# Performance work log

Hardware: AMD Instinct MI355X
Metric: run time of the kernel (lower is better)

## Reference

```python
import jax, jax.numpy as jnp
import numpy as np

N_NODES = 100000
N_EDGES = 1600000
NFEAT, NHID, NCLASS = 256, 512, 256


def _init_params(key):
    ks = jax.random.split(key, 8)
    s = 0.02
    p = {
        'W1a': jax.random.normal(ks[0], (NFEAT, NHID), jnp.float32) * s,
        'b1a': jnp.zeros((NHID,), jnp.float32),
        'W1b': jax.random.normal(ks[1], (NHID, NHID), jnp.float32) * s,
        'b1b': jnp.zeros((NHID,), jnp.float32),
        'W2a': jax.random.normal(ks[2], (NHID, NHID), jnp.float32) * s,
        'b2a': jnp.zeros((NHID,), jnp.float32),
        'W2b': jax.random.normal(ks[3], (NHID, NCLASS), jnp.float32) * s,
        'b2b': jnp.zeros((NCLASS,), jnp.float32),
        'eps1': jnp.zeros((), jnp.float32),
        'eps2': jnp.zeros((), jnp.float32),
    }
    return p


def setup_inputs() -> dict:
    key = jax.random.key(0)
    kx, ke, kp = jax.random.split(key, 3)
    x = jax.random.normal(kx, (N_NODES, NFEAT), jnp.float32)
    edge_index = jax.random.randint(ke, (2, N_EDGES), 0, N_NODES, jnp.int64)
    inp = {'x': x, 'edge_index': edge_index}
    inp.update(_init_params(kp))
    return inp


def _gin_agg(h, src, dst, eps, n_nodes):
    # sum of neighbor (source) features at each destination node + (1+eps)*self
    agg = jax.ops.segment_sum(h[src], dst, num_segments=n_nodes)
    return (1.0 + eps) * h + agg


def reference(x, edge_index, W1a, b1a, W1b, b1b, W2a, b2a, W2b, b2b, eps1, eps2):
    src, dst = edge_index[0], edge_index[1]
    n = x.shape[0]
    # GINConv layer 1: MLP = Linear-ReLU-Linear-ReLU
    h = _gin_agg(x, src, dst, eps1, n)
    h = jax.nn.relu(h @ W1a + b1a)
    h = jax.nn.relu(h @ W1b + b1b)
    # dropout: eval mode (identity)
    # GINConv layer 2: MLP = Linear-ReLU-Linear
    h = _gin_agg(h, src, dst, eps2, n)
    h = jax.nn.relu(h @ W2a + b2a)
    out = h @ W2b + b2b
    return out
```

## Files before the change

kernel.cpp:

```cpp
#include <hip/hip_runtime.h>
#include <hip/hip_bf16.h>
#include <stdint.h>

#define NN 100000
#define NFEATD 256
#define NHIDD 512
#define NCLASSD 256

typedef short bf16x8 __attribute__((ext_vector_type(8)));
typedef float f32x4 __attribute__((ext_vector_type(4)));
typedef float f32x2 __attribute__((ext_vector_type(2)));

__device__ __forceinline__ float bf2f(uint32_t u) {
    union { uint32_t i; float f; } v; v.i = u << 16; return v.f;
}
__device__ __forceinline__ ushort f2bf(float f) {
    uint32_t x = __float_as_uint(f);
    uint32_t r = (x + 0x7FFF + ((x >> 16) & 1)) >> 16;
    return (ushort)r;
}

__global__ void zero_i32(int* __restrict__ p, int n) {
    int i = blockIdx.x * 256 + threadIdx.x;
    if (i < n) p[i] = 0;
}

__global__ void count_deg(const int* __restrict__ dst, int* __restrict__ deg, int nE) {
    int e = blockIdx.x * 256 + threadIdx.x;
    if (e < nE) atomicAdd(&deg[dst[e]], 1);
}

__global__ __launch_bounds__(1024) void scan_excl(const int* __restrict__ deg,
                                                  int* __restrict__ off, int n) {
    __shared__ int wsum[16];
    __shared__ int carry_s;
    const int tid = threadIdx.x;
    const int lane = tid & 63, wv = tid >> 6;
    if (tid == 0) carry_s = 0;
    __syncthreads();
    for (int base = 0; base < n; base += 1024) {
        int i = base + tid;
        int v = (i < n) ? deg[i] : 0;
        int x = v;
#pragma unroll
        for (int d = 1; d < 64; d <<= 1) {
            int y = __shfl_up(x, d, 64);
            if (lane >= d) x += y;
        }
        if (lane == 63) wsum[wv] = x;
        __syncthreads();
        if (wv == 0 && lane < 16) {
            int s = wsum[lane];
#pragma unroll
            for (int d = 1; d < 16; d <<= 1) {
                int y = __shfl_up(s, d, 16);
                if (lane >= d) s += y;
            }
            wsum[lane] = s;
        }
        __syncthreads();
        int carry = carry_s;
        int wprefix = (wv == 0) ? 0 : wsum[wv - 1];
        if (i < n) off[i] = carry + wprefix + x - v;
        __syncthreads();
        if (tid == 0) carry_s = carry + wsum[15];
        __syncthreads();
    }
    if (tid == 0) off[n] = carry_s;
}

__global__ void fill_csr(const int* __restrict__ src, const int* __restrict__ dst,
                         const int* __restrict__ off, int* __restrict__ cursor,
                         int* __restrict__ csr, int nE) {
    int e = blockIdx.x * 256 + threadIdx.x;
    if (e >= nE) return;
    int d = dst[e];
    int p = off[d] + atomicAdd(&cursor[d], 1);
    csr[p] = src[e];
}

__global__ void prep_w4(const float* __restrict__ W1a, const float* __restrict__ W1b,
                        const float* __restrict__ W2a, const float* __restrict__ W2b,
                        ushort* __restrict__ Wt1a, ushort* __restrict__ Wt1b,
                        ushort* __restrict__ Wt2a, ushort* __restrict__ Wt2b) {
    int idx = blockIdx.x * 256 + threadIdx.x;
    if (idx < 131072) {
        int k = idx >> 9, n = idx & 511;
        Wt1a[n * 256 + k] = f2bf(W1a[idx]);
    } else if (idx < 131072 + 262144) {
        int i = idx - 131072;
        int k = i >> 9, n = i & 511;
        Wt1b[n * 512 + k] = f2bf(W1b[i]);
    } else if (idx < 131072 + 524288) {
        int i = idx - (131072 + 262144);
        int k = i >> 9, n = i & 511;
        Wt2a[n * 512 + k] = f2bf(W2a[i]);
    } else if (idx < 131072 + 524288 + 131072) {
        int i = idx - (131072 + 524288);
        int k = i >> 8, n = i & 255;
        Wt2b[n * 512 + k] = f2bf(W2b[i]);
    }
}

__global__ void cast_f32_fp8(const float* __restrict__ a, uint8_t* __restrict__ o, int n) {
    int i = (blockIdx.x * 256 + threadIdx.x) * 8;
    if (i >= n) return;
    float4 v0 = *(const float4*)(a + i);
    float4 v1 = *(const float4*)(a + i + 4);
    int lo = __builtin_amdgcn_cvt_pk_fp8_f32(v0.x, v0.y, 0, false);
    lo = __builtin_amdgcn_cvt_pk_fp8_f32(v0.z, v0.w, lo, true);
    int hi = __builtin_amdgcn_cvt_pk_fp8_f32(v1.x, v1.y, 0, false);
    hi = __builtin_amdgcn_cvt_pk_fp8_f32(v1.z, v1.w, hi, true);
    uint2 r; r.x = (uint32_t)lo; r.y = (uint32_t)hi;
    *(uint2*)(o + i) = r;
}

__device__ __forceinline__ void accp(uint32_t p, f32x2& lo, f32x2& hi) {
    lo += __builtin_amdgcn_cvt_pk_f32_fp8((int)p, false);
    hi += __builtin_amdgcn_cvt_pk_f32_fp8((int)p, true);
}

__global__ void gather256f8(const uint8_t* __restrict__ X8, const int* __restrict__ off,
                            const int* __restrict__ csr, const float* __restrict__ eps,
                            ushort* __restrict__ out) {
    int node = (blockIdx.x * 256 + threadIdx.x) >> 6;
    if (node >= NN) return;
    int lane = threadIdx.x & 63;
    float sc = 1.0f + *eps;
    f32x2 scv = {sc, sc};
    const uint32_t* X1 = (const uint32_t*)X8;
    f32x2 lo = {0.f, 0.f}, hi = {0.f, 0.f};
    {
        uint32_t p = X1[(size_t)node * 64 + lane];
        lo = scv * __builtin_amdgcn_cvt_pk_f32_fp8((int)p, false);
        hi = scv * __builtin_amdgcn_cvt_pk_f32_fp8((int)p, true);
    }
    int e = off[node], e1 = off[node + 1];
    for (; e + 7 < e1; e += 8) {
        uint32_t p[8];
#pragma unroll
        for (int t = 0; t < 8; ++t) p[t] = X1[(size_t)csr[e + t] * 64 + lane];
#pragma unroll
        for (int t = 0; t < 8; ++t) accp(p[t], lo, hi);
    }
    for (; e < e1; ++e)
        accp(X1[(size_t)csr[e] * 64 + lane], lo, hi);
    uint2 r;
    r.x = (uint32_t)f2bf(lo[0]) | ((uint32_t)f2bf(lo[1]) << 16);
    r.y = (uint32_t)f2bf(hi[0]) | ((uint32_t)f2bf(hi[1]) << 16);
    *(uint2*)(out + (size_t)node * 256 + lane * 4) = r;
}

__global__ void gather512f8(const uint8_t* __restrict__ H8, const int* __restrict__ off,
                            const int* __restrict__ csr, const float* __restrict__ eps,
                            ushort* __restrict__ out) {
    int node = (blockIdx.x * 256 + threadIdx.x) >> 6;
    if (node >= NN) return;
    int lane = threadIdx.x & 63;
    float sc = 1.0f + *eps;
    f32x2 scv = {sc, sc};
    const uint2* H2 = (const uint2*)H8;
    f32x2 l0 = {0.f, 0.f}, h0 = {0.f, 0.f}, l1 = {0.f, 0.f}, h1 = {0.f, 0.f};
    {
        uint2 p = H2[(size_t)node * 64 + lane];
        l0 = scv * __builtin_amdgcn_cvt_pk_f32_fp8((int)p.x, false);
        h0 = scv * __builtin_amdgcn_cvt_pk_f32_fp8((int)p.x, true);
        l1 = scv * __builtin_amdgcn_cvt_pk_f32_fp8((int)p.y, false);
        h1 = scv * __builtin_amdgcn_cvt_pk_f32_fp8((int)p.y, true);
    }
    int e = off[node], e1 = off[node + 1];
    for (; e + 7 < e1; e += 8) {
        uint2 p[8];
#pragma unroll
        for (int t = 0; t < 8; ++t) p[t] = H2[(size_t)csr[e + t] * 64 + lane];
#pragma unroll
        for (int t = 0; t < 8; ++t) {
            accp(p[t].x, l0, h0);
            accp(p[t].y, l1, h1);
        }
    }
    for (; e < e1; ++e) {
        uint2 p = H2[(size_t)csr[e] * 64 + lane];
        accp(p.x, l0, h0);
        accp(p.y, l1, h1);
    }
    uint4 r;
    r.x = (uint32_t)f2bf(l0[0]) | ((uint32_t)f2bf(l0[1]) << 16);
    r.y = (uint32_t)f2bf(h0[0]) | ((uint32_t)f2bf(h0[1]) << 16);
    r.z = (uint32_t)f2bf(l1[0]) | ((uint32_t)f2bf(l1[1]) << 16);
    r.w = (uint32_t)f2bf(h1[0]) | ((uint32_t)f2bf(h1[1]) << 16);
    *(uint4*)(out + (size_t)node * 512 + lane * 8) = r;
}


__device__ __forceinline__ void stage_a(const ushort* __restrict__ A, int K, int row0,
                                        int kc, ushort* dst, int tid, int Mm1) {
    int r = tid >> 2, c = tid & 3;
    int gr = row0 + r; if (gr > Mm1) gr = Mm1;
    const ushort* gp = A + (size_t)gr * K + kc + c * 8;
    __builtin_amdgcn_global_load_lds((const __attribute__((address_space(1))) void*)gp,
        (__attribute__((address_space(3))) void*)(dst + tid * 8), 16, 0, 0);
}

__device__ __forceinline__ void stage_b(const ushort* __restrict__ Bt, int K, int col0,
                                        int kc, ushort* dst, int tid) {
#pragma unroll
    for (int i = 0; i < 2; ++i) {
        int u = i * 512 + tid;
        int r = u >> 2, c = u & 3;
        const ushort* gp = Bt + (size_t)(col0 + r) * K + kc + c * 8;
        __builtin_amdgcn_global_load_lds((const __attribute__((address_space(1))) void*)gp,
            (__attribute__((address_space(3))) void*)(dst + u * 8), 16, 0, 0);
    }
}

__global__ __launch_bounds__(512, 4) void gemm_bt(
    const ushort* __restrict__ A, const ushort* __restrict__ Bt,
    const float* __restrict__ bias, float* __restrict__ outf,
    uint8_t* __restrict__ out8, ushort* __restrict__ outb,
    int M, int N, int K, int relu)
{
    __shared__ ushort smem[2][12288];
    const int tid = threadIdx.x;
    const int wave = tid >> 6, lane = tid & 63;
    const int quad = lane >> 4, lrow = lane & 15;
    const int wr = wave >> 2, wcn = wave & 3;
    const int row0 = blockIdx.y * 128, col0 = blockIdx.x * 256;
    const int NC = K >> 5;

    f32x4 acc[4][4] = {};

    stage_a(A, K, row0, 0, smem[0], tid, M - 1);
    stage_b(Bt, K, col0, 0, smem[0] + 4096, tid);
    __syncthreads();

    for (int t = 0; t < NC; ++t) {
        const ushort* As = smem[t & 1];
        const ushort* Bs = As + 4096;
        if (t + 1 < NC) {
            stage_a(A, K, row0, (t + 1) << 5, smem[(t + 1) & 1], tid, M - 1);
            stage_b(Bt, K, col0, (t + 1) << 5, smem[(t + 1) & 1] + 4096, tid);
        }
        bf16x8 af[4], bfr[4];
#pragma unroll
        for (int m = 0; m < 4; ++m)
            af[m] = *(const bf16x8*)(As + (wr * 64 + m * 16 + lrow) * 32 + quad * 8);
#pragma unroll
        for (int n = 0; n < 4; ++n)
            bfr[n] = *(const bf16x8*)(Bs + (wcn * 64 + n * 16 + lrow) * 32 + quad * 8);
        __builtin_amdgcn_s_setprio(1);
#pragma unroll
        for (int m = 0; m < 4; ++m)
#pragma unroll
            for (int n = 0; n < 4; ++n)
                acc[m][n] = __builtin_amdgcn_mfma_f32_16x16x32_bf16(bfr[n], af[m], acc[m][n], 0, 0, 0);
        __builtin_amdgcn_s_setprio(0);
        __syncthreads();
    }

#pragma unroll
    for (int m = 0; m < 4; ++m) {
        int rr = row0 + wr * 64 + m * 16 + lrow;
        if (rr < M) {
#pragma unroll
            for (int n = 0; n < 4; ++n) {
                int c = col0 + wcn * 64 + n * 16 + quad * 4;
                float4 bv = *(const float4*)(bias + c);
                float v0 = acc[m][n][0] + bv.x;
                float v1 = acc[m][n][1] + bv.y;
                float v2 = acc[m][n][2] + bv.z;
                float v3 = acc[m][n][3] + bv.w;
                if (relu) {
                    v0 = fmaxf(v0, 0.f); v1 = fmaxf(v1, 0.f);
                    v2 = fmaxf(v2, 0.f); v3 = fmaxf(v3, 0.f);
                }
                if (outf) {
                    float4 o; o.x = v0; o.y = v1; o.z = v2; o.w = v3;
                    *(float4*)(outf + (size_t)rr * N + c) = o;
                } else if (out8) {
                    int enc = __builtin_amdgcn_cvt_pk_fp8_f32(v0, v1, 0, false);
                    enc = __builtin_amdgcn_cvt_pk_fp8_f32(v2, v3, enc, true);
                    *(uint32_t*)(out8 + (size_t)rr * N + c) = (uint32_t)enc;
                } else {
                    uint2 o;
                    o.x = (uint32_t)f2bf(v0) | ((uint32_t)f2bf(v1) << 16);
                    o.y = (uint32_t)f2bf(v2) | ((uint32_t)f2bf(v3) << 16);
                    *(uint2*)(outb + (size_t)rr * N + c) = o;
                }
            }
        }
    }
}

extern "C" void kernel_launch(void* const* d_in, const int* in_sizes, int n_in,
                              void* d_out, int out_size, void* d_ws, size_t ws_size,
                              hipStream_t stream) {
    const float* x    = (const float*)d_in[0];
    const int*   ei   = (const int*)d_in[1];
    const float* W1a  = (const float*)d_in[2];
    const float* b1a  = (const float*)d_in[3];
    const float* W1b  = (const float*)d_in[4];
    const float* b1b  = (const float*)d_in[5];
    const float* W2a  = (const float*)d_in[6];
    const float* b2a  = (const float*)d_in[7];
    const float* W2b  = (const float*)d_in[8];
    const float* b2b  = (const float*)d_in[9];
    const float* eps1 = (const float*)d_in[10];
    const float* eps2 = (const float*)d_in[11];
    const int nE = in_sizes[1] / 2;
    const int* srcv = ei;
    const int* dstv = ei + nE;

    char* ws = (char*)d_ws;
    int*    off    = (int*)(ws);
    int*    cursor = (int*)(ws + 524288);
    int*    csr    = (int*)(ws + 1048576);
    ushort* Wt1a   = (ushort*)(ws + 8388608);
    ushort* Wt1b   = Wt1a + 512 * 256;
    ushort* Wt2a   = Wt1b + 512 * 512;
    ushort* Wt2b   = Wt2a + 512 * 512;
    char*   P      = ws + 10485760;
    char*   Q      = ws + 10485760 + 102400000;
    uint8_t* x8    = (uint8_t*)P;
    ushort* agg1b  = (ushort*)Q;
    ushort* h1     = (ushort*)P;
    uint8_t* h2f8  = (uint8_t*)Q;
    ushort* agg2b  = (ushort*)P;
    ushort* h3     = (ushort*)Q;

    zero_i32<<<(NN + 255) / 256, 256, 0, stream>>>(cursor, NN);
    count_deg<<<(nE + 255) / 256, 256, 0, stream>>>(dstv, cursor, nE);
    scan_excl<<<1, 1024, 0, stream>>>(cursor, off, NN);
    zero_i32<<<(NN + 255) / 256, 256, 0, stream>>>(cursor, NN);
    fill_csr<<<(nE + 255) / 256, 256, 0, stream>>>(srcv, dstv, off, cursor, csr, nE);

    prep_w4<<<(786432 + 255) / 256, 256, 0, stream>>>(W1a, W1b, W2a, W2b,
                                                      Wt1a, Wt1b, Wt2a, Wt2b);
    cast_f32_fp8<<<(NN * NFEATD / 8 + 255) / 256, 256, 0, stream>>>(x, x8, NN * NFEATD);

    gather256f8<<<(NN * 64) / 256, 256, 0, stream>>>(x8, off, csr, eps1, agg1b);
    dim3 g1(NHIDD / 256, (NN + 127) / 128);
    gemm_bt<<<g1, 512, 0, stream>>>(agg1b, Wt1a, b1a, nullptr, nullptr, h1, NN, NHIDD, NFEATD, 1);
    gemm_bt<<<g1, 512, 0, stream>>>(h1, Wt1b, b1b, nullptr, h2f8, nullptr, NN, NHIDD, NHIDD, 1);

    gather512f8<<<(NN * 64) / 256, 256, 0, stream>>>(h2f8, off, csr, eps2, agg2b);
    gemm_bt<<<g1, 512, 0, stream>>>(agg2b, Wt2a, b2a, nullptr, nullptr, h3, NN, NHIDD, NHIDD, 1);
    dim3 g2(NCLASSD / 256, (NN + 127) / 128);
    gemm_bt<<<g2, 512, 0, stream>>>(h3, Wt2b, b2b, (float*)d_out, nullptr, nullptr, NN, NCLASSD, NHIDD, 0);
}
```

Before: 927.4 us.

## Load B fragments directly to registers and shrink GEMM tile to 128x128

The GEMM kernel now stages only the A tile in LDS and has each wave load its B (weight) fragments straight from global memory into registers. The loop is unrolled by two with ping-pong register and LDS buffers. The block tile shrinks from 128x256 with 512 threads to 128x128 with 256 threads, which cuts LDS use and allows more resident blocks. In exchange, A tiles are re-read by twice as many column blocks, and B global loads go to registers without LDS sharing across waves, so global traffic for B rises.

New measurement: 1.153 ms. +24.3%, slower.

```diff
diff --git a/kernel.cpp b/kernel.cpp
--- a/kernel.cpp
+++ b/kernel.cpp
@@ -193,67 +193,77 @@
 }
 
 
-__device__ __forceinline__ void stage_a(const ushort* __restrict__ A, int K, int row0,
-                                        int kc, ushort* dst, int tid, int Mm1) {
-    int r = tid >> 2, c = tid & 3;
-    int gr = row0 + r; if (gr > Mm1) gr = Mm1;
-    const ushort* gp = A + (size_t)gr * K + kc + c * 8;
-    __builtin_amdgcn_global_load_lds((const __attribute__((address_space(1))) void*)gp,
-        (__attribute__((address_space(3))) void*)(dst + tid * 8), 16, 0, 0);
-}
-
-__device__ __forceinline__ void stage_b(const ushort* __restrict__ Bt, int K, int col0,
-                                        int kc, ushort* dst, int tid) {
+__device__ __forceinline__ void stage_a256(const ushort* __restrict__ A, int K, int row0,
+                                           int kc, ushort* dst, int tid, int Mm1) {
 #pragma unroll
     for (int i = 0; i < 2; ++i) {
-        int u = i * 512 + tid;
+        int u = i * 256 + tid;
         int r = u >> 2, c = u & 3;
-        const ushort* gp = Bt + (size_t)(col0 + r) * K + kc + c * 8;
+        int gr = row0 + r; if (gr > Mm1) gr = Mm1;
+        const ushort* gp = A + (size_t)gr * K + kc + c * 8;
         __builtin_amdgcn_global_load_lds((const __attribute__((address_space(1))) void*)gp,
             (__attribute__((address_space(3))) void*)(dst + u * 8), 16, 0, 0);
     }
 }
 
-__global__ __launch_bounds__(512, 4) void gemm_bt(
+__global__ __launch_bounds__(256, 4) void gemm_bt(
     const ushort* __restrict__ A, const ushort* __restrict__ Bt,
     const float* __restrict__ bias, float* __restrict__ outf,
     uint8_t* __restrict__ out8, ushort* __restrict__ outb,
     int M, int N, int K, int relu)
 {
-    __shared__ ushort smem[2][12288];
+    __shared__ ushort As[2][4096];
     const int tid = threadIdx.x;
     const int wave = tid >> 6, lane = tid & 63;
     const int quad = lane >> 4, lrow = lane & 15;
-    const int wr = wave >> 2, wcn = wave & 3;
-    const int row0 = blockIdx.y * 128, col0 = blockIdx.x * 256;
+    const int wr = wave >> 1, wc = wave & 1;
+    const int row0 = blockIdx.y * 128, col0 = blockIdx.x * 128;
     const int NC = K >> 5;
 
     f32x4 acc[4][4] = {};
-
-    stage_a(A, K, row0, 0, smem[0], tid, M - 1);
-    stage_b(Bt, K, col0, 0, smem[0] + 4096, tid);
+    bf16x8 bA[4], bB[4], af[4];
+
+    const ushort* bbase = Bt + (size_t)(col0 + wc * 64 + lrow) * K + quad * 8;
+
+    stage_a256(A, K, row0, 0, As[0], tid, M - 1);
+#pragma unroll
+    for (int n = 0; n < 4; ++n) bA[n] = *(const bf16x8*)(bbase + n * 16 * K);
     __syncthreads();
 
-    for (int t = 0; t < NC; ++t) {
-        const ushort* As = smem[t & 1];
-        const ushort* Bs = As + 4096;
-        if (t + 1 < NC) {
-            stage_a(A, K, row0, (t + 1) << 5, smem[(t + 1) & 1], tid, M - 1);
-            stage_b(Bt, K, col0, (t + 1) << 5, smem[(t + 1) & 1] + 4096, tid);
-        }
-        bf16x8 af[4], bfr[4];
+    for (int t = 0; t < NC; t += 2) {
+        {
+            int kn = (t + 1) << 5;
+            stage_a256(A, K, row0, kn, As[1], tid, M - 1);
+#pragma unroll
+            for (int n = 0; n < 4; ++n) bB[n] = *(const bf16x8*)(bbase + n * 16 * K + kn);
+        }
 #pragma unroll
         for (int m = 0; m < 4; ++m)
-            af[m] = *(const bf16x8*)(As + (wr * 64 + m * 16 + lrow) * 32 + quad * 8);
-#pragma unroll
-        for (int n = 0; n < 4; ++n)
-            bfr[n] = *(const bf16x8*)(Bs + (wcn * 64 + n * 16 + lrow) * 32 + quad * 8);
+            af[m] = *(const bf16x8*)(As[0] + (wr * 64 + m * 16 + lrow) * 32 + quad * 8);
         __builtin_amdgcn_s_setprio(1);
 #pragma unroll
         for (int m = 0; m < 4; ++m)
 #pragma unroll
             for (int n = 0; n < 4; ++n)
-                acc[m][n] = __builtin_amdgcn_mfma_f32_16x16x32_bf16(bfr[n], af[m], acc[m][n], 0, 0, 0);
+                acc[m][n] = __builtin_amdgcn_mfma_f32_16x16x32_bf16(bA[n], af[m], acc[m][n], 0, 0, 0);
+        __builtin_amdgcn_s_setprio(0);
+        __syncthreads();
+
+        if (t + 2 < NC) {
+            int kn = (t + 2) << 5;
+            stage_a256(A, K, row0, kn, As[0], tid, M - 1);
+#pragma unroll
+            for (int n = 0; n < 4; ++n) bA[n] = *(const bf16x8*)(bbase + n * 16 * K + kn);
+        }
+#pragma unroll
+        for (int m = 0; m < 4; ++m)
+            af[m] = *(const bf16x8*)(As[1] + (wr * 64 + m * 16 + lrow) * 32 + quad * 8);
+        __builtin_amdgcn_s_setprio(1);
+#pragma unroll
+        for (int m = 0; m < 4; ++m)
+#pragma unroll
+            for (int n = 0; n < 4; ++n)
+                acc[m][n] = __builtin_amdgcn_mfma_f32_16x16x32_bf16(bB[n], af[m], acc[m][n], 0, 0, 0);
         __builtin_amdgcn_s_setprio(0);
         __syncthreads();
     }
@@ -264,7 +274,7 @@
         if (rr < M) {
 #pragma unroll
             for (int n = 0; n < 4; ++n) {
-                int c = col0 + wcn * 64 + n * 16 + quad * 4;
+                int c = col0 + wc * 64 + n * 16 + quad * 4;
                 float4 bv = *(const float4*)(bias + c);
                 float v0 = acc[m][n][0] + bv.x;
                 float v1 = acc[m][n][1] + bv.y;
@@ -339,12 +349,12 @@
     cast_f32_fp8<<<(NN * NFEATD / 8 + 255) / 256, 256, 0, stream>>>(x, x8, NN * NFEATD);
 
     gather256f8<<<(NN * 64) / 256, 256, 0, stream>>>(x8, off, csr, eps1, agg1b);
-    dim3 g1(NHIDD / 256, (NN + 127) / 128);
-    gemm_bt<<<g1, 512, 0, stream>>>(agg1b, Wt1a, b1a, nullptr, nullptr, h1, NN, NHIDD, NFEATD, 1);
-    gemm_bt<<<g1, 512, 0, stream>>>(h1, Wt1b, b1b, nullptr, h2f8, nullptr, NN, NHIDD, NHIDD, 1);
+    dim3 g1(NHIDD / 128, (NN + 127) / 128);
+    gemm_bt<<<g1, 256, 0, stream>>>(agg1b, Wt1a, b1a, nullptr, nullptr, h1, NN, NHIDD, NFEATD, 1);
+    gemm_bt<<<g1, 256, 0, stream>>>(h1, Wt1b, b1b, nullptr, h2f8, nullptr, NN, NHIDD, NHIDD, 1);
 
     gather512f8<<<(NN * 64) / 256, 256, 0, stream>>>(h2f8, off, csr, eps2, agg2b);
-    gemm_bt<<<g1, 512, 0, stream>>>(agg2b, Wt2a, b2a, nullptr, nullptr, h3, NN, NHIDD, NHIDD, 1);
-    dim3 g2(NCLASSD / 256, (NN + 127) / 128);
-    gemm_bt<<<g2, 512, 0, stream>>>(h3, Wt2b, b2b, (float*)d_out, nullptr, nullptr, NN, NCLASSD, NHIDD, 0);
-}
+    gemm_bt<<<g1, 256, 0, stream>>>(agg2b, Wt2a, b2a, nullptr, nullptr, h3, NN, NHIDD, NHIDD, 1);
+    dim3 g2(NCLASSD / 128, (NN + 127) / 128);
+    gemm_bt<<<g2, 256, 0, stream>>>(h3, Wt2b, b2b, (float*)d_out, nullptr, nullptr, NN, NCLASSD, NHIDD, 0);
+}
```
